# Performance work log

Hardware: AMD Instinct MI355X
Metric: run time of the kernel (lower is better)

Reference implementation:

```python
import jax, jax.numpy as jnp
import numpy as np

N, E, F, H, ED, C, G = 50000, 800000, 86, 128, 16, 18, 64
NEG_SLOPE = 0.2


def setup_inputs() -> dict:
    key = jax.random.key(0)
    ks = jax.random.split(key, 20)
    s = 0.1
    return {
        "x": jax.random.normal(ks[0], (N, F), jnp.float32),
        "edge_index": jax.random.randint(ks[1], (2, E), 0, N, jnp.int32),
        "edge_attr": jax.random.normal(ks[2], (E, ED), jnp.float32),
        "batch": jnp.sort(jax.random.randint(ks[3], (N,), 0, G, jnp.int32)),
        # conv1 params (GATConv, heads=1): lin, lin_edge (no bias), att vectors, bias
        "W1": jax.random.normal(ks[4], (F, H), jnp.float32) * s,
        "We1": jax.random.normal(ks[5], (ED, H), jnp.float32) * s,
        "as1": jax.random.normal(ks[6], (H,), jnp.float32) * s,
        "ad1": jax.random.normal(ks[7], (H,), jnp.float32) * s,
        "ae1": jax.random.normal(ks[8], (H,), jnp.float32) * s,
        "b1": jnp.zeros((H,), jnp.float32),
        # conv2 params
        "W2": jax.random.normal(ks[9], (H, H), jnp.float32) * s,
        "We2": jax.random.normal(ks[10], (ED, H), jnp.float32) * s,
        "as2": jax.random.normal(ks[11], (H,), jnp.float32) * s,
        "ad2": jax.random.normal(ks[12], (H,), jnp.float32) * s,
        "ae2": jax.random.normal(ks[13], (H,), jnp.float32) * s,
        "b2": jnp.zeros((H,), jnp.float32),
        # final classifier
        "Wl": jax.random.normal(ks[14], (H, C), jnp.float32) * s,
        "bl": jnp.zeros((C,), jnp.float32),
    }


def gat_conv(x, edge_attr, src, dst, W, We, a_src, a_dst, a_edge, bias):
    h = x @ W                                   # [N, H]
    e = edge_attr @ We                          # [E, H]
    # per-edge attention logits: a_src.h_j + a_dst.h_i + a_edge.e
    alpha = (h @ a_src)[src] + (h @ a_dst)[dst] + e @ a_edge   # [E]
    alpha = jax.nn.leaky_relu(alpha, NEG_SLOPE)
    # segment softmax over incoming edges of each destination node
    m = jax.ops.segment_max(alpha, dst, num_segments=N)
    ex = jnp.exp(alpha - m[dst])
    denom = jax.ops.segment_sum(ex, dst, num_segments=N)
    w = ex / jnp.maximum(denom[dst], 1e-16)     # [E]
    out = jax.ops.segment_sum(h[src] * w[:, None], dst, num_segments=N)
    return out + bias


def reference(x, edge_index, edge_attr, batch,
              W1, We1, as1, ad1, ae1, b1,
              W2, We2, as2, ad2, ae2, b2,
              Wl, bl):
    src, dst = edge_index[0], edge_index[1]
    h = jax.nn.relu(gat_conv(x, edge_attr, src, dst, W1, We1, as1, ad1, ae1, b1))
    h = jax.nn.relu(gat_conv(h, edge_attr, src, dst, W2, We2, as2, ad2, ae2, b2))
    pooled = jax.ops.segment_max(h, batch, num_segments=G)      # [G, H] global max pool
    pooled = jnp.where(jnp.isfinite(pooled), pooled, 0.0)       # guard empty graphs
    logits = pooled @ Wl + bl                                   # [G, C]
    return jax.nn.log_softmax(logits, axis=-1)
```

## Files before the change

### kernel.cpp

```cpp
#include <hip/hip_runtime.h>
#include <math.h>

#define N_NODES 50000
#define N_EDGES 800000
#define F_IN    86
#define H_DIM   128
#define ED_DIM  16
#define C_CLS   18
#define G_GRAPHS 64
#define NEG_SLOPE 0.2f
#define SCAN_BLOCKS ((N_NODES + 255) / 256)
#define EB_BLOCKS ((N_EDGES + 255) / 256)
#define GB_BLOCKS ((N_NODES + 63) / 64)

typedef _Float16 h2v   __attribute__((ext_vector_type(2)));
typedef _Float16 half8 __attribute__((ext_vector_type(8)));
typedef float    f4v   __attribute__((ext_vector_type(4)));
typedef unsigned long long ull;

__device__ __forceinline__ void atomicMaxFloat(float* addr, float val) {
    if (val >= 0.0f) atomicMax((int*)addr, __float_as_int(val));
    else             atomicMin((unsigned int*)addr, __float_as_uint(val));
}

__global__ void prep(int* __restrict__ cnt, float* __restrict__ pooled,
                     const float* __restrict__ We1, const float* __restrict__ ae1,
                     const float* __restrict__ We2, const float* __restrict__ ae2,
                     float* __restrict__ ve1, float* __restrict__ ve2) {
    int b = blockIdx.x, t = threadIdx.x;
    if (b < SCAN_BLOCKS) {
        int i = b * 256 + t;
        if (i < N_NODES) cnt[i] = 0;
    } else {
        if (t < ED_DIM) {
            float s = 0.f;
            for (int h = 0; h < H_DIM; ++h) s += We1[t * H_DIM + h] * ae1[h];
            ve1[t] = s;
        } else if (t < 2 * ED_DIM) {
            int j = t - ED_DIM;
            float s = 0.f;
            for (int h = 0; h < H_DIM; ++h) s += We2[j * H_DIM + h] * ae2[h];
            ve2[j] = s;
        }
        for (int i = t; i < G_GRAPHS * H_DIM; i += 256) pooled[i] = 0.f;
    }
}

__global__ void hist_rank_dots(const int* __restrict__ dst, int* __restrict__ cnt,
                               unsigned short* __restrict__ rank,
                               const float* __restrict__ ea,
                               const float* __restrict__ ve1, const float* __restrict__ ve2,
                               unsigned int* __restrict__ dotp) {
    int e = blockIdx.x * blockDim.x + threadIdx.x;
    if (e >= N_EDGES) return;
    int r = atomicAdd(&cnt[dst[e]], 1);
    rank[e] = (unsigned short)r;
    const float4* p = (const float4*)(ea + (size_t)e * ED_DIM);
    float4 v0 = p[0], v1 = p[1], v2 = p[2], v3 = p[3];
    float s1 = v0.x*ve1[0] + v0.y*ve1[1] + v0.z*ve1[2] + v0.w*ve1[3]
             + v1.x*ve1[4] + v1.y*ve1[5] + v1.z*ve1[6] + v1.w*ve1[7]
             + v2.x*ve1[8] + v2.y*ve1[9] + v2.z*ve1[10] + v2.w*ve1[11]
             + v3.x*ve1[12] + v3.y*ve1[13] + v3.z*ve1[14] + v3.w*ve1[15];
    float s2 = v0.x*ve2[0] + v0.y*ve2[1] + v0.z*ve2[2] + v0.w*ve2[3]
             + v1.x*ve2[4] + v1.y*ve2[5] + v1.z*ve2[6] + v1.w*ve2[7]
             + v2.x*ve2[8] + v2.y*ve2[9] + v2.z*ve2[10] + v2.w*ve2[11]
             + v3.x*ve2[12] + v3.y*ve2[13] + v3.z*ve2[14] + v3.w*ve2[15];
    h2v dv;
    dv.x = (_Float16)s1;
    dv.y = (_Float16)s2;
    dotp[e] = __builtin_bit_cast(unsigned int, dv);
}

__global__ void scan1(const int* __restrict__ cnt, int* __restrict__ excl,
                      int* __restrict__ bsum) {
    __shared__ int s[256];
    int tid = threadIdx.x;
    int i = blockIdx.x * 256 + tid;
    int v = (i < N_NODES) ? cnt[i] : 0;
    s[tid] = v;
    __syncthreads();
    for (int o = 1; o < 256; o <<= 1) {
        int t = (tid >= o) ? s[tid - o] : 0;
        __syncthreads();
        s[tid] += t;
        __syncthreads();
    }
    if (i < N_NODES) excl[i] = s[tid] - v;
    if (tid == 255) bsum[blockIdx.x] = s[255];
}

__global__ void scan23(const int* __restrict__ excl, const int* __restrict__ bsum,
                       int* __restrict__ row_ptr) {
    __shared__ int s[256];
    int tid = threadIdx.x;
    int v = (tid < SCAN_BLOCKS) ? bsum[tid] : 0;
    s[tid] = v;
    __syncthreads();
    for (int o = 1; o < 256; o <<= 1) {
        int t = (tid >= o) ? s[tid - o] : 0;
        __syncthreads();
        s[tid] += t;
        __syncthreads();
    }
    int boff = s[blockIdx.x] - bsum[blockIdx.x];
    int i = blockIdx.x * 256 + tid;
    if (i < N_NODES) row_ptr[i] = excl[i] + boff;
    if (i == 0) row_ptr[N_NODES] = N_EDGES;
}

__global__ void scatter_lite(const int* __restrict__ src, const int* __restrict__ dst,
                             const int* __restrict__ row_ptr,
                             const unsigned short* __restrict__ rank,
                             const unsigned int* __restrict__ dotp,
                             int2* __restrict__ perm) {
    int e = blockIdx.x * blockDim.x + threadIdx.x;
    if (e >= N_EDGES) return;
    int pos = row_ptr[dst[e]] + rank[e];
    perm[pos] = make_int2(src[e], (int)dotp[e]);
}

#define KP1 104
__global__ __launch_bounds__(256)
void gemm1(const float* __restrict__ in, const float* __restrict__ W,
           const float* __restrict__ a_s, const float* __restrict__ a_d,
           _Float16* __restrict__ hout, float* __restrict__ hs, float* __restrict__ hd) {
    __shared__ __attribute__((aligned(16))) _Float16 Asm[64 * KP1];
    __shared__ __attribute__((aligned(16))) _Float16 Bsm[128 * KP1];
    __shared__ float sdots[64][2][2];
    int tid = threadIdx.x;
    int n0 = blockIdx.x * 64;

    const float2* in2 = (const float2*)(in + (size_t)n0 * F_IN);
    for (int idx = tid; idx < 64 * (F_IN / 2); idx += 256) {
        int r = idx / (F_IN / 2), k2 = idx - r * (F_IN / 2);
        float2 v = (n0 + r < N_NODES) ? in2[idx] : make_float2(0.f, 0.f);
        Asm[r * KP1 + 2 * k2]     = (_Float16)v.x;
        Asm[r * KP1 + 2 * k2 + 1] = (_Float16)v.y;
    }
    for (int idx = tid; idx < 64 * (96 - F_IN); idx += 256) {
        int r = idx / (96 - F_IN), k = F_IN + idx - r * (96 - F_IN);
        Asm[r * KP1 + k] = (_Float16)0.f;
    }
    const float4* W4 = (const float4*)W;
    for (int idx = tid; idx < F_IN * 32; idx += 256) {
        float4 v = W4[idx];
        int k = idx >> 5, n = (idx & 31) * 4;
        Bsm[(n + 0) * KP1 + k] = (_Float16)v.x;
        Bsm[(n + 1) * KP1 + k] = (_Float16)v.y;
        Bsm[(n + 2) * KP1 + k] = (_Float16)v.z;
        Bsm[(n + 3) * KP1 + k] = (_Float16)v.w;
    }
    for (int idx = tid; idx < 128 * (96 - F_IN); idx += 256) {
        int n = idx / (96 - F_IN), k = F_IN + idx - n * (96 - F_IN);
        Bsm[n * KP1 + k] = (_Float16)0.f;
    }
    __syncthreads();

    int wave = tid >> 6, lane = tid & 63;
    int wm = (wave & 1) * 32, wn = (wave >> 1) * 64;
    int m16 = lane & 15, quad = lane >> 4;

    f4v acc[2][4];
#pragma unroll
    for (int t = 0; t < 2; ++t)
#pragma unroll
        for (int c = 0; c < 4; ++c) acc[t][c] = (f4v){0.f, 0.f, 0.f, 0.f};

#pragma unroll
    for (int kk = 0; kk < 96 / 32; ++kk) {
        int koff = kk * 32 + quad * 8;
        half8 a0 = *(const half8*)&Asm[(wm + m16) * KP1 + koff];
        half8 a1 = *(const half8*)&Asm[(wm + 16 + m16) * KP1 + koff];
#pragma unroll
        for (int c = 0; c < 4; ++c) {
            half8 b = *(const half8*)&Bsm[(wn + c * 16 + m16) * KP1 + koff];
            acc[0][c] = __builtin_amdgcn_mfma_f32_16x16x32_f16(a0, b, acc[0][c], 0, 0, 0);
            acc[1][c] = __builtin_amdgcn_mfma_f32_16x16x32_f16(a1, b, acc[1][c], 0, 0, 0);
        }
    }

    float asv[4], adv[4];
#pragma unroll
    for (int c = 0; c < 4; ++c) {
        asv[c] = a_s[wn + c * 16 + m16];
        adv[c] = a_d[wn + c * 16 + m16];
    }
#pragma unroll
    for (int t = 0; t < 2; ++t)
#pragma unroll
        for (int r = 0; r < 4; ++r) {
            float ps = 0.f, pd = 0.f;
#pragma unroll
            for (int c = 0; c < 4; ++c) {
                float v = acc[t][c][r];
                ps += v * asv[c];
                pd += v * adv[c];
            }
#pragma unroll
            for (int o = 1; o < 16; o <<= 1) {
                ps += __shfl_xor(ps, o);
                pd += __shfl_xor(pd, o);
            }
            if (m16 == 0) {
                int row = wm + t * 16 + quad * 4 + r;
                sdots[row][wn >> 6][0] = ps;
                sdots[row][wn >> 6][1] = pd;
            }
        }
#pragma unroll
    for (int t = 0; t < 2; ++t)
#pragma unroll
        for (int c = 0; c < 4; ++c)
#pragma unroll
            for (int r = 0; r < 4; ++r) {
                int row = n0 + wm + t * 16 + quad * 4 + r;
                if (row < N_NODES)
                    hout[(size_t)row * H_DIM + wn + c * 16 + m16] = (_Float16)acc[t][c][r];
            }
    __syncthreads();
    if (tid < 64) {
        int row = n0 + tid;
        if (row < N_NODES) {
            hs[row] = sdots[tid][0][0] + sdots[tid][1][0];
            hd[row] = sdots[tid][0][1] + sdots[tid][1][1];
        }
    }
}

#define KP2 136
__global__ __launch_bounds__(256)
void gemm2(const _Float16* __restrict__ in, const float* __restrict__ W,
           const float* __restrict__ a_s, const float* __restrict__ a_d,
           _Float16* __restrict__ hout, float* __restrict__ hs, float* __restrict__ hd) {
    __shared__ __attribute__((aligned(16))) _Float16 Asm[64 * KP2];
    __shared__ __attribute__((aligned(16))) _Float16 Bsm[128 * KP2];
    __shared__ float sdots[64][2][2];
    int tid = threadIdx.x;
    int n0 = blockIdx.x * 64;

    const half8* in8 = (const half8*)(in + (size_t)n0 * H_DIM);
    for (int idx = tid; idx < 64 * 16; idx += 256) {
        int r = idx >> 4, k8 = idx & 15;
        half8 v = (n0 + r < N_NODES) ? in8[idx]
                                     : (half8){0, 0, 0, 0, 0, 0, 0, 0};
        *(half8*)&Asm[r * KP2 + k8 * 8] = v;
    }
    const float4* W4 = (const float4*)W;
    for (int idx = tid; idx < 128 * 32; idx += 256) {
        float4 v = W4[idx];
        int k = idx >> 5, n = (idx & 31) * 4;
        Bsm[(n + 0) * KP2 + k] = (_Float16)v.x;
        Bsm[(n + 1) * KP2 + k] = (_Float16)v.y;
        Bsm[(n + 2) * KP2 + k] = (_Float16)v.z;
        Bsm[(n + 3) * KP2 + k] = (_Float16)v.w;
    }
    __syncthreads();

    int wave = tid >> 6, lane = tid & 63;
    int wm = (wave & 1) * 32, wn = (wave >> 1) * 64;
    int m16 = lane & 15, quad = lane >> 4;

    f4v acc[2][4];
#pragma unroll
    for (int t = 0; t < 2; ++t)
#pragma unroll
        for (int c = 0; c < 4; ++c) acc[t][c] = (f4v){0.f, 0.f, 0.f, 0.f};

#pragma unroll
    for (int kk = 0; kk < 128 / 32; ++kk) {
        int koff = kk * 32 + quad * 8;
        half8 a0 = *(const half8*)&Asm[(wm + m16) * KP2 + koff];
        half8 a1 = *(const half8*)&Asm[(wm + 16 + m16) * KP2 + koff];
#pragma unroll
        for (int c = 0; c < 4; ++c) {
            half8 b = *(const half8*)&Bsm[(wn + c * 16 + m16) * KP2 + koff];
            acc[0][c] = __builtin_amdgcn_mfma_f32_16x16x32_f16(a0, b, acc[0][c], 0, 0, 0);
            acc[1][c] = __builtin_amdgcn_mfma_f32_16x16x32_f16(a1, b, acc[1][c], 0, 0, 0);
        }
    }

    float asv[4], adv[4];
#pragma unroll
    for (int c = 0; c < 4; ++c) {
        asv[c] = a_s[wn + c * 16 + m16];
        adv[c] = a_d[wn + c * 16 + m16];
    }
#pragma unroll
    for (int t = 0; t < 2; ++t)
#pragma unroll
        for (int r = 0; r < 4; ++r) {
            float ps = 0.f, pd = 0.f;
#pragma unroll
            for (int c = 0; c < 4; ++c) {
                float v = acc[t][c][r];
                ps += v * asv[c];
                pd += v * adv[c];
            }
#pragma unroll
            for (int o = 1; o < 16; o <<= 1) {
                ps += __shfl_xor(ps, o);
                pd += __shfl_xor(pd, o);
            }
            if (m16 == 0) {
                int row = wm + t * 16 + quad * 4 + r;
                sdots[row][wn >> 6][0] = ps;
                sdots[row][wn >> 6][1] = pd;
            }
        }
#pragma unroll
    for (int t = 0; t < 2; ++t)
#pragma unroll
        for (int c = 0; c < 4; ++c)
#pragma unroll
            for (int r = 0; r < 4; ++r) {
                int row = n0 + wm + t * 16 + quad * 4 + r;
                if (row < N_NODES)
                    hout[(size_t)row * H_DIM + wn + c * 16 + m16] = (_Float16)acc[t][c][r];
            }
    __syncthreads();
    if (tid < 64) {
        int row = n0 + tid;
        if (row < N_NODES) {
            hs[row] = sdots[tid][0][0] + sdots[tid][1][0];
            hd[row] = sdots[tid][0][1] + sdots[tid][1][1];
        }
    }
}

template<int DOT, bool POOL>
__global__ void gat_node(const int* __restrict__ row_ptr, const int2* __restrict__ perm,
                         const float* __restrict__ hs, const float* __restrict__ hd,
                         const _Float16* __restrict__ h, const float* __restrict__ bias,
                         _Float16* __restrict__ out,
                         const int* __restrict__ batch, float* __restrict__ pooled) {
    __shared__ float smax[H_DIM];
    __shared__ int sg[4];
    __shared__ __attribute__((aligned(16))) ull stage[4][64];
    int tid = threadIdx.x;
    if (POOL) {
        if (tid < H_DIM) smax[tid] = 0.f;
        __syncthreads();
    }
    int n = blockIdx.x * 4 + (tid >> 6);
    int lane = tid & 63;
    int q = lane >> 4, m = lane & 15;
    int r0 = row_ptr[n], r1 = row_ptr[n + 1];
    float hdn = hd[n];
    const char* hb = (const char*)h;
    unsigned mo = (unsigned)(m * 16);
    ull* st = stage[tid >> 6];

    float acc[8];
#pragma unroll
    for (int k = 0; k < 8; ++k) acc[k] = 0.f;
    float denl = 0.f;

    for (int c = r0; c < r1; c += 64) {
        int i = c + lane;
        float w = 0.f;
        int so = 0;
        if (i < r1) {
            int2 p = perm[i];
            so = p.x * (H_DIM * 2);
            h2v dv = __builtin_bit_cast(h2v, p.y);
            float dotv = (DOT == 1) ? (float)dv.x : (float)dv.y;
            float t = hs[p.x] + hdn + dotv;
            t = (t > 0.f) ? t : NEG_SLOPE * t;
            w = __expf(t);
        }
        denl += w;
        st[lane] = (ull)(unsigned)so | ((ull)__float_as_uint(w) << 32);
        int lim = r1 - c; if (lim > 64) lim = 64;
        int njj = (lim + 7) >> 3;
        int jj = 0;
        for (; jj + 2 <= njj; jj += 2) {
            int b8 = jj << 3;
            ull p1 = st[b8 + q];
            ull p2 = st[b8 + q + 4];
            ull p3 = st[b8 + q + 8];
            ull p4 = st[b8 + q + 12];
            float w1 = __uint_as_float((unsigned)(p1 >> 32));
            float w2 = __uint_as_float((unsigned)(p2 >> 32));
            float w3 = __uint_as_float((unsigned)(p3 >> 32));
            float w4 = __uint_as_float((unsigned)(p4 >> 32));
            half8 v1 = *(const half8*)(hb + ((unsigned)p1 + mo));
            half8 v2 = *(const half8*)(hb + ((unsigned)p2 + mo));
            half8 v3 = *(const half8*)(hb + ((unsigned)p3 + mo));
            half8 v4 = *(const half8*)(hb + ((unsigned)p4 + mo));
#pragma unroll
            for (int k = 0; k < 8; ++k) acc[k] += w1 * (float)v1[k];
#pragma unroll
            for (int k = 0; k < 8; ++k) acc[k] += w2 * (float)v2[k];
#pragma unroll
            for (int k = 0; k < 8; ++k) acc[k] += w3 * (float)v3[k];
#pragma unroll
            for (int k = 0; k < 8; ++k) acc[k] += w4 * (float)v4[k];
        }
        if (jj < njj) {
            int b8 = jj << 3;
            ull p1 = st[b8 + q];
            ull p2 = st[b8 + q + 4];
            float w1 = __uint_as_float((unsigned)(p1 >> 32));
            float w2 = __uint_as_float((unsigned)(p2 >> 32));
            half8 v1 = *(const half8*)(hb + ((unsigned)p1 + mo));
            half8 v2 = *(const half8*)(hb + ((unsigned)p2 + mo));
#pragma unroll
            for (int k = 0; k < 8; ++k) acc[k] += w1 * (float)v1[k];
#pragma unroll
            for (int k = 0; k < 8; ++k) acc[k] += w2 * (float)v2[k];
        }
    }
#pragma unroll
    for (int k = 0; k < 8; ++k) {
        acc[k] += __shfl_xor(acc[k], 16);
        acc[k] += __shfl_xor(acc[k], 32);
    }
    float den = denl;
#pragma unroll
    for (int o = 32; o > 0; o >>= 1) den += __shfl_xor(den, o);
    float inv = 1.f / fmaxf(den, 1e-16f);

    float rv[8];
    if (q == 0) {
        float4 b0 = ((const float4*)bias)[2 * m];
        float4 b1 = ((const float4*)bias)[2 * m + 1];
        rv[0] = fmaxf(acc[0] * inv + b0.x, 0.f);
        rv[1] = fmaxf(acc[1] * inv + b0.y, 0.f);
        rv[2] = fmaxf(acc[2] * inv + b0.z, 0.f);
        rv[3] = fmaxf(acc[3] * inv + b0.w, 0.f);
        rv[4] = fmaxf(acc[4] * inv + b1.x, 0.f);
        rv[5] = fmaxf(acc[5] * inv + b1.y, 0.f);
        rv[6] = fmaxf(acc[6] * inv + b1.z, 0.f);
        rv[7] = fmaxf(acc[7] * inv + b1.w, 0.f);
    }

    if (!POOL) {
        if (q == 0) {
            half8 ov;
#pragma unroll
            for (int k = 0; k < 8; ++k) ov[k] = (_Float16)rv[k];
            *(half8*)&out[(size_t)n * H_DIM + m * 8] = ov;
        }
    } else {
        int g = batch[n];
        if (lane == 0) sg[tid >> 6] = g;
        if (q == 0) {
#pragma unroll
            for (int k = 0; k < 8; ++k)
                atomicMax((int*)&smax[m * 8 + k], __float_as_int(rv[k]));
        }
        __syncthreads();
        if (sg[0] == sg[3]) {
            if (tid < H_DIM)
                atomicMaxFloat(&pooled[sg[0] * H_DIM + tid], smax[tid]);
        } else {
            if (q == 0) {
#pragma unroll
                for (int k = 0; k < 8; ++k)
                    atomicMaxFloat(&pooled[g * H_DIM + m * 8 + k], rv[k]);
            }
        }
    }
}

__global__ void final_logits(const float* __restrict__ pooled, const float* __restrict__ Wl,
                             const float* __restrict__ bl, float* __restrict__ outp) {
    int g = threadIdx.x;
    if (g >= G_GRAPHS) return;
    float lg[C_CLS];
#pragma unroll
    for (int c = 0; c < C_CLS; ++c) lg[c] = bl[c];
    for (int k = 0; k < H_DIM; ++k) {
        float v = pooled[g * H_DIM + k];
#pragma unroll
        for (int c = 0; c < C_CLS; ++c) lg[c] += v * Wl[k * C_CLS + c];
    }
    float mx = lg[0];
#pragma unroll
    for (int c = 1; c < C_CLS; ++c) mx = fmaxf(mx, lg[c]);
    float se = 0.f;
#pragma unroll
    for (int c = 0; c < C_CLS; ++c) se += expf(lg[c] - mx);
    float lse = logf(se);
#pragma unroll
    for (int c = 0; c < C_CLS; ++c) outp[g * C_CLS + c] = lg[c] - mx - lse;
}

extern "C" void kernel_launch(void* const* d_in, const int* in_sizes, int n_in,
                              void* d_out, int out_size, void* d_ws, size_t ws_size,
                              hipStream_t stream) {
    const float* x     = (const float*)d_in[0];
    const int*   eidx  = (const int*)d_in[1];
    const float* ea    = (const float*)d_in[2];
    const int*   batch = (const int*)d_in[3];
    const float* W1  = (const float*)d_in[4];
    const float* We1 = (const float*)d_in[5];
    const float* as1 = (const float*)d_in[6];
    const float* ad1 = (const float*)d_in[7];
    const float* ae1 = (const float*)d_in[8];
    const float* b1  = (const float*)d_in[9];
    const float* W2  = (const float*)d_in[10];
    const float* We2 = (const float*)d_in[11];
    const float* as2 = (const float*)d_in[12];
    const float* ad2 = (const float*)d_in[13];
    const float* ae2 = (const float*)d_in[14];
    const float* b2  = (const float*)d_in[15];
    const float* Wl  = (const float*)d_in[16];
    const float* bl  = (const float*)d_in[17];
    float* outp = (float*)d_out;

    const int* src = eidx;
    const int* dst = eidx + N_EDGES;

    char* wsb = (char*)d_ws;
    size_t off = 0;
    auto alloc = [&](size_t bytes) { char* p = wsb + off; off += (bytes + 255) & ~(size_t)255; return p; };
    _Float16* h    = (_Float16*)alloc((size_t)N_NODES * H_DIM * 2);
    _Float16* A2   = (_Float16*)alloc((size_t)N_NODES * H_DIM * 2);
    int2*  perm    = (int2*)alloc((size_t)N_EDGES * 8);
    unsigned short* rank = (unsigned short*)alloc((size_t)N_EDGES * 2);
    unsigned int* dotp = (unsigned int*)alloc((size_t)N_EDGES * 4);
    float* hs      = (float*)alloc(N_NODES * 4);
    float* hd      = (float*)alloc(N_NODES * 4);
    int*   row_ptr = (int*)alloc((N_NODES + 1) * 4);
    int*   cnt     = (int*)alloc(N_NODES * 4);
    int*   excl    = (int*)alloc(N_NODES * 4);
    int*   bsum    = (int*)alloc(SCAN_BLOCKS * 4);
    float* pooled  = (float*)alloc(G_GRAPHS * H_DIM * 4);
    float* ve1     = (float*)alloc(16 * 4);
    float* ve2     = (float*)alloc(16 * 4);

    const int NB4 = (N_NODES + 3) / 4;

    prep<<<SCAN_BLOCKS + 1, 256, 0, stream>>>(cnt, pooled, We1, ae1, We2, ae2, ve1, ve2);
    hist_rank_dots<<<EB_BLOCKS, 256, 0, stream>>>(dst, cnt, rank, ea, ve1, ve2, dotp);
    scan1<<<SCAN_BLOCKS, 256, 0, stream>>>(cnt, excl, bsum);
    scan23<<<SCAN_BLOCKS, 256, 0, stream>>>(excl, bsum, row_ptr);
    scatter_lite<<<EB_BLOCKS, 256, 0, stream>>>(src, dst, row_ptr, rank, dotp, perm);

    gemm1<<<GB_BLOCKS, 256, 0, stream>>>(x, W1, as1, ad1, h, hs, hd);
    gat_node<1, false><<<NB4, 256, 0, stream>>>(row_ptr, perm, hs, hd, h, b1, A2,
                                                batch, pooled);

    gemm2<<<GB_BLOCKS, 256, 0, stream>>>(A2, W2, as2, ad2, h, hs, hd);
    gat_node<2, true><<<NB4, 256, 0, stream>>>(row_ptr, perm, hs, hd, h, b2, nullptr,
                                               batch, pooled);

    final_logits<<<1, 64, 0, stream>>>(pooled, Wl, bl, outp);
}
```

Baseline: 320.6 us.

## Fuse edge histogram into gemm1 launch and fold final logits into last gat block

The edge histogram/rank/dot kernel is merged into the gemm1 launch as extra blocks, each handling four edges per thread, so the independent GEMM and edge work can run concurrently in one grid. The final logits kernel is removed and its work is done by the last finishing block of the second gat_node, detected through an atomic done counter with thread fences. This removes two launches and lets independent work overlap. The cost is heavier contention on the done atomic and a serial tail in one block.

```diff
diff --git a/kernel.cpp b/kernel.cpp
--- a/kernel.cpp
+++ b/kernel.cpp
@@ -12,6 +12,8 @@
 #define SCAN_BLOCKS ((N_NODES + 255) / 256)
 #define EB_BLOCKS ((N_EDGES + 255) / 256)
 #define GB_BLOCKS ((N_NODES + 63) / 64)
+#define HB_BLOCKS 782
+#define HB_THREADS (HB_BLOCKS * 256)
 
 typedef _Float16 h2v   __attribute__((ext_vector_type(2)));
 typedef _Float16 half8 __attribute__((ext_vector_type(8)));
@@ -26,7 +28,8 @@
 __global__ void prep(int* __restrict__ cnt, float* __restrict__ pooled,
                      const float* __restrict__ We1, const float* __restrict__ ae1,
                      const float* __restrict__ We2, const float* __restrict__ ae2,
-                     float* __restrict__ ve1, float* __restrict__ ve2) {
+                     float* __restrict__ ve1, float* __restrict__ ve2,
+                     int* __restrict__ done) {
     int b = blockIdx.x, t = threadIdx.x;
     if (b < SCAN_BLOCKS) {
         int i = b * 256 + t;
@@ -42,33 +45,9 @@
             for (int h = 0; h < H_DIM; ++h) s += We2[j * H_DIM + h] * ae2[h];
             ve2[j] = s;
         }
+        if (t == 255) *done = 0;
         for (int i = t; i < G_GRAPHS * H_DIM; i += 256) pooled[i] = 0.f;
     }
-}
-
-__global__ void hist_rank_dots(const int* __restrict__ dst, int* __restrict__ cnt,
-                               unsigned short* __restrict__ rank,
-                               const float* __restrict__ ea,
-                               const float* __restrict__ ve1, const float* __restrict__ ve2,
-                               unsigned int* __restrict__ dotp) {
-    int e = blockIdx.x * blockDim.x + threadIdx.x;
-    if (e >= N_EDGES) return;
-    int r = atomicAdd(&cnt[dst[e]], 1);
-    rank[e] = (unsigned short)r;
-    const float4* p = (const float4*)(ea + (size_t)e * ED_DIM);
-    float4 v0 = p[0], v1 = p[1], v2 = p[2], v3 = p[3];
-    float s1 = v0.x*ve1[0] + v0.y*ve1[1] + v0.z*ve1[2] + v0.w*ve1[3]
-             + v1.x*ve1[4] + v1.y*ve1[5] + v1.z*ve1[6] + v1.w*ve1[7]
-             + v2.x*ve1[8] + v2.y*ve1[9] + v2.z*ve1[10] + v2.w*ve1[11]
-             + v3.x*ve1[12] + v3.y*ve1[13] + v3.z*ve1[14] + v3.w*ve1[15];
-    float s2 = v0.x*ve2[0] + v0.y*ve2[1] + v0.z*ve2[2] + v0.w*ve2[3]
-             + v1.x*ve2[4] + v1.y*ve2[5] + v1.z*ve2[6] + v1.w*ve2[7]
-             + v2.x*ve2[8] + v2.y*ve2[9] + v2.z*ve2[10] + v2.w*ve2[11]
-             + v3.x*ve2[12] + v3.y*ve2[13] + v3.z*ve2[14] + v3.w*ve2[15];
-    h2v dv;
-    dv.x = (_Float16)s1;
-    dv.y = (_Float16)s2;
-    dotp[e] = __builtin_bit_cast(unsigned int, dv);
 }
 
 __global__ void scan1(const int* __restrict__ cnt, int* __restrict__ excl,
@@ -121,15 +100,46 @@
 
 #define KP1 104
 __global__ __launch_bounds__(256)
-void gemm1(const float* __restrict__ in, const float* __restrict__ W,
-           const float* __restrict__ a_s, const float* __restrict__ a_d,
-           _Float16* __restrict__ hout, float* __restrict__ hs, float* __restrict__ hd) {
+void gemm1_hist(const float* __restrict__ in, const float* __restrict__ W,
+                const float* __restrict__ a_s, const float* __restrict__ a_d,
+                _Float16* __restrict__ hout, float* __restrict__ hs, float* __restrict__ hd,
+                const int* __restrict__ dst, int* __restrict__ cnt,
+                unsigned short* __restrict__ rank, const float* __restrict__ ea,
+                const float* __restrict__ ve1, const float* __restrict__ ve2,
+                unsigned int* __restrict__ dotp) {
     __shared__ __attribute__((aligned(16))) _Float16 Asm[64 * KP1];
     __shared__ __attribute__((aligned(16))) _Float16 Bsm[128 * KP1];
     __shared__ float sdots[64][2][2];
     int tid = threadIdx.x;
+
+    if (blockIdx.x >= GB_BLOCKS) {
+        int tbase = (blockIdx.x - GB_BLOCKS) * 256 + tid;
+#pragma unroll
+        for (int u = 0; u < 4; ++u) {
+            int e = tbase + u * HB_THREADS;
+            if (e < N_EDGES) {
+                int r = atomicAdd(&cnt[dst[e]], 1);
+                rank[e] = (unsigned short)r;
+                const float4* p = (const float4*)(ea + (size_t)e * ED_DIM);
+                float4 v0 = p[0], v1 = p[1], v2 = p[2], v3 = p[3];
+                float s1 = v0.x*ve1[0] + v0.y*ve1[1] + v0.z*ve1[2] + v0.w*ve1[3]
+                         + v1.x*ve1[4] + v1.y*ve1[5] + v1.z*ve1[6] + v1.w*ve1[7]
+                         + v2.x*ve1[8] + v2.y*ve1[9] + v2.z*ve1[10] + v2.w*ve1[11]
+                         + v3.x*ve1[12] + v3.y*ve1[13] + v3.z*ve1[14] + v3.w*ve1[15];
+                float s2 = v0.x*ve2[0] + v0.y*ve2[1] + v0.z*ve2[2] + v0.w*ve2[3]
+                         + v1.x*ve2[4] + v1.y*ve2[5] + v1.z*ve2[6] + v1.w*ve2[7]
+                         + v2.x*ve2[8] + v2.y*ve2[9] + v2.z*ve2[10] + v2.w*ve2[11]
+                         + v3.x*ve2[12] + v3.y*ve2[13] + v3.z*ve2[14] + v3.w*ve2[15];
+                h2v dv;
+                dv.x = (_Float16)s1;
+                dv.y = (_Float16)s2;
+                dotp[e] = __builtin_bit_cast(unsigned int, dv);
+            }
+        }
+        return;
+    }
+
     int n0 = blockIdx.x * 64;
-
     const float2* in2 = (const float2*)(in + (size_t)n0 * F_IN);
     for (int idx = tid; idx < 64 * (F_IN / 2); idx += 256) {
         int r = idx / (F_IN / 2), k2 = idx - r * (F_IN / 2);
@@ -332,9 +342,12 @@
                          const float* __restrict__ hs, const float* __restrict__ hd,
                          const _Float16* __restrict__ h, const float* __restrict__ bias,
                          _Float16* __restrict__ out,
-                         const int* __restrict__ batch, float* __restrict__ pooled) {
+                         const int* __restrict__ batch, float* __restrict__ pooled,
+                         const float* __restrict__ Wl, const float* __restrict__ bl,
+                         float* __restrict__ outp, int* __restrict__ done) {
     __shared__ float smax[H_DIM];
     __shared__ int sg[4];
+    __shared__ int slast;
     __shared__ __attribute__((aligned(16))) ull stage[4][64];
     int tid = threadIdx.x;
     if (POOL) {
@@ -460,30 +473,33 @@
                     atomicMaxFloat(&pooled[g * H_DIM + m * 8 + k], rv[k]);
             }
         }
-    }
-}
-
-__global__ void final_logits(const float* __restrict__ pooled, const float* __restrict__ Wl,
-                             const float* __restrict__ bl, float* __restrict__ outp) {
-    int g = threadIdx.x;
-    if (g >= G_GRAPHS) return;
-    float lg[C_CLS];
-#pragma unroll
-    for (int c = 0; c < C_CLS; ++c) lg[c] = bl[c];
-    for (int k = 0; k < H_DIM; ++k) {
-        float v = pooled[g * H_DIM + k];
-#pragma unroll
-        for (int c = 0; c < C_CLS; ++c) lg[c] += v * Wl[k * C_CLS + c];
-    }
-    float mx = lg[0];
-#pragma unroll
-    for (int c = 1; c < C_CLS; ++c) mx = fmaxf(mx, lg[c]);
-    float se = 0.f;
-#pragma unroll
-    for (int c = 0; c < C_CLS; ++c) se += expf(lg[c] - mx);
-    float lse = logf(se);
-#pragma unroll
-    for (int c = 0; c < C_CLS; ++c) outp[g * C_CLS + c] = lg[c] - mx - lse;
+        __threadfence();
+        if (tid == 0) slast = atomicAdd(done, 1);
+        __syncthreads();
+        if (slast == (int)gridDim.x - 1) {
+            __threadfence();
+            if (tid < G_GRAPHS) {
+                int gg = tid;
+                float lg[C_CLS];
+#pragma unroll
+                for (int c = 0; c < C_CLS; ++c) lg[c] = bl[c];
+                for (int k = 0; k < H_DIM; ++k) {
+                    float v = __int_as_float(atomicMax((int*)&pooled[gg * H_DIM + k], 0));
+#pragma unroll
+                    for (int c = 0; c < C_CLS; ++c) lg[c] += v * Wl[k * C_CLS + c];
+                }
+                float mx = lg[0];
+#pragma unroll
+                for (int c = 1; c < C_CLS; ++c) mx = fmaxf(mx, lg[c]);
+                float se = 0.f;
+#pragma unroll
+                for (int c = 0; c < C_CLS; ++c) se += expf(lg[c] - mx);
+                float lse = logf(se);
+#pragma unroll
+                for (int c = 0; c < C_CLS; ++c) outp[gg * C_CLS + c] = lg[c] - mx - lse;
+            }
+        }
+    }
 }
 
 extern "C" void kernel_launch(void* const* d_in, const int* in_sizes, int n_in,
@@ -529,22 +545,21 @@
     float* pooled  = (float*)alloc(G_GRAPHS * H_DIM * 4);
     float* ve1     = (float*)alloc(16 * 4);
     float* ve2     = (float*)alloc(16 * 4);
+    int*   done    = (int*)alloc(4);
 
     const int NB4 = (N_NODES + 3) / 4;
 
-    prep<<<SCAN_BLOCKS + 1, 256, 0, stream>>>(cnt, pooled, We1, ae1, We2, ae2, ve1, ve2);
-    hist_rank_dots<<<EB_BLOCKS, 256, 0, stream>>>(dst, cnt, rank, ea, ve1, ve2, dotp);
+    prep<<<SCAN_BLOCKS + 1, 256, 0, stream>>>(cnt, pooled, We1, ae1, We2, ae2, ve1, ve2, done);
+    gemm1_hist<<<GB_BLOCKS + HB_BLOCKS, 256, 0, stream>>>(x, W1, as1, ad1, h, hs, hd,
+                                                          dst, cnt, rank, ea, ve1, ve2, dotp);
     scan1<<<SCAN_BLOCKS, 256, 0, stream>>>(cnt, excl, bsum);
     scan23<<<SCAN_BLOCKS, 256, 0, stream>>>(excl, bsum, row_ptr);
     scatter_lite<<<EB_BLOCKS, 256, 0, stream>>>(src, dst, row_ptr, rank, dotp, perm);
 
-    gemm1<<<GB_BLOCKS, 256, 0, stream>>>(x, W1, as1, ad1, h, hs, hd);
     gat_node<1, false><<<NB4, 256, 0, stream>>>(row_ptr, perm, hs, hd, h, b1, A2,
-                                                batch, pooled);
+                                                batch, pooled, nullptr, nullptr, nullptr, nullptr);
 
     gemm2<<<GB_BLOCKS, 256, 0, stream>>>(A2, W2, as2, ad2, h, hs, hd);
     gat_node<2, true><<<NB4, 256, 0, stream>>>(row_ptr, perm, hs, hd, h, b2, nullptr,
-                                               batch, pooled);
-
-    final_logits<<<1, 64, 0, stream>>>(pooled, Wl, bl, outp);
-}
+                                               batch, pooled, Wl, bl, outp, done);
+}
```

Result: slower. 1.250 ms (+290.0%).
